# Kernel tuning notes

Measured on AMD Instinct MI355X. Metric: run time of the kernel, lower is better.

Reference implementation:

```python
import jax, jax.numpy as jnp
import numpy as np

N, E, D = 50000, 1200000, 64
NEG_SLOPE = 0.2  # PyG GATConv LeakyReLU slope
EPS_SM = 1e-16   # PyG softmax eps
EPS_LN = 1e-5


def _glorot(key, shape):
    fan = shape[0]
    return jax.random.normal(key, shape, jnp.float32) / np.float32(np.sqrt(fan))


def setup_inputs() -> dict:
    key = jax.random.key(0)
    ks = jax.random.split(key, 16)
    inp = {
        "x": jax.random.normal(ks[0], (N, D), jnp.float32),
        "edge_index": jax.random.randint(ks[1], (2, E), 0, N, dtype=jnp.int32),
        # layer 0: bipartite-style (-1,-1) GATConv -> separate src/dst projections
        "W_src0": _glorot(ks[2], (D, D)), "W_dst0": _glorot(ks[3], (D, D)),
        "a_src0": _glorot(ks[4], (D,)), "a_dst0": _glorot(ks[5], (D,)),
        "b0": jnp.zeros((D,), jnp.float32),
        "lin_W0": _glorot(ks[6], (D, D)), "lin_b0": jnp.zeros((D,), jnp.float32),
        # layers 1,2: int in_channels -> shared projection for src and dst
        "W1": _glorot(ks[7], (D, D)),
        "a_src1": _glorot(ks[8], (D,)), "a_dst1": _glorot(ks[9], (D,)),
        "b1": jnp.zeros((D,), jnp.float32),
        "lin_W1": _glorot(ks[10], (D, D)), "lin_b1": jnp.zeros((D,), jnp.float32),
        "W2": _glorot(ks[11], (D, D)),
        "a_src2": _glorot(ks[12], (D,)), "a_dst2": _glorot(ks[13], (D,)),
        "b2": jnp.zeros((D,), jnp.float32),
        "lin_W2": _glorot(ks[14], (D, D)), "lin_b2": jnp.zeros((D,), jnp.float32),
        "ln_w": jnp.ones((D,), jnp.float32), "ln_b": jnp.zeros((D,), jnp.float32),
        "proj_W": _glorot(ks[15], (D, 1)), "proj_b": jnp.zeros((1,), jnp.float32),
    }
    return inp


def _gat(x_src, x_dst, a_src, a_dst, bias, src, dst):
    # per-edge attention logit: a_src.x_j + a_dst.x_i, LeakyReLU
    alpha = (x_src * a_src).sum(-1)[src] + (x_dst * a_dst).sum(-1)[dst]  # [E]
    alpha = jnp.where(alpha >= 0, alpha, NEG_SLOPE * alpha)
    # segment softmax over edges sharing a destination node
    m = jax.ops.segment_max(alpha, dst, num_segments=N)
    m = jnp.where(jnp.isfinite(m), m, 0.0)  # empty segments -> -inf -> 0
    e = jnp.exp(alpha - m[dst])
    denom = jax.ops.segment_sum(e, dst, num_segments=N)
    w = e / (denom[dst] + EPS_SM)
    # weighted scatter-add aggregation
    return jax.ops.segment_sum(w[:, None] * x_src[src], dst, num_segments=N) + bias


def reference(x, edge_index,
              W_src0, W_dst0, a_src0, a_dst0, b0, lin_W0, lin_b0,
              W1, a_src1, a_dst1, b1, lin_W1, lin_b1,
              W2, a_src2, a_dst2, b2, lin_W2, lin_b2,
              ln_w, ln_b, proj_W, proj_b):
    src, dst = edge_index[0], edge_index[1]
    h = _gat(x @ W_src0, x @ W_dst0, a_src0, a_dst0, b0, src, dst) + x @ lin_W0 + lin_b0
    h = jax.nn.relu(h)
    hp = h @ W1
    h = _gat(hp, hp, a_src1, a_dst1, b1, src, dst) + h @ lin_W1 + lin_b1
    h = jax.nn.relu(h)
    hp = h @ W2
    h = _gat(hp, hp, a_src2, a_dst2, b2, src, dst) + h @ lin_W2 + lin_b2
    # PyG LayerNorm mode='graph': normalize over all nodes and channels
    mu = h.mean()
    var = h.var()
    h = (h - mu) * jax.lax.rsqrt(var + EPS_LN) * ln_w + ln_b
    return h @ proj_W + proj_b  # [N, 1]
```

## Files before the change

### kernel.cpp

```cpp
#include <hip/hip_runtime.h>
#include <hip/hip_bf16.h>

#define NN 50000
#define NE 1200000
#define D 64
#define NEG_SLOPE 0.2f
#define EPS_SM 1e-16f
#define EPS_LN 1e-5f
#define KMAX 4
#define PIPE 8
#define BSH 6
#define NBUK 782
#define BCAP 2048
#define BCAPSH 11
#define EPB 4096
#define NPB 293
#define GEMM_BLOCKS 3125
#define GAT_BLOCKS 12500

typedef __attribute__((ext_vector_type(8))) short short8;
typedef __attribute__((ext_vector_type(4))) float float4v;

__device__ __forceinline__ float waveReduceSum(float v) {
    #pragma unroll
    for (int off = 32; off > 0; off >>= 1)
        v += __shfl_xor(v, off, 64);
    return v;
}
__device__ __forceinline__ float bflo(unsigned v) { return __uint_as_float(v << 16); }
__device__ __forceinline__ float bfhi(unsigned v) { return __uint_as_float(v & 0xffff0000u); }
__device__ __forceinline__ short f2bf_bits(float f) {
    __hip_bfloat16 b = __float2bfloat16(f);
    short v; __builtin_memcpy(&v, &b, 2);
    return v;
}

struct WP7 { const float* p[7]; };

__global__ __launch_bounds__(256) void pack_w7(WP7 wp, unsigned short* __restrict__ wpk) {
    const int n = 7 * 4096;
    for (int idx = blockIdx.x * 256 + threadIdx.x; idx < n; idx += gridDim.x * 256) {
        const int j = idx & 7;
        const int lane = (idx >> 3) & 63;
        const int khtile = idx >> 9;
        const int kh = khtile & 1;
        const int tile = khtile >> 1;
        const int mat = tile >> 2;
        const int ch = (tile & 3) * 16 + (lane & 15);
        const int k = kh * 32 + (lane >> 4) * 8 + j;
        wpk[idx] = (unsigned short)f2bf_bits(wp.p[mat][k * D + ch]);
    }
}

template <int NMATS>
__global__ __launch_bounds__(256) void gemm_mfma(
                          const float* __restrict__ hin,
                          const unsigned short* __restrict__ wpk,
                          const float* __restrict__ avs,
                          const float* __restrict__ avd,
                          const float* __restrict__ bgat,
                          const float* __restrict__ blin,
                          __hip_bfloat16* __restrict__ hp,
                          float* __restrict__ agg,
                          float* __restrict__ alpha_s,
                          float* __restrict__ alpha_d) {
    constexpr int NT   = NMATS * 4;
    constexpr int NTPW = NT / 4;
    __shared__ float xt[16 * D];
    __shared__ float ared[2][4][16];

    const int t   = threadIdx.x;
    const int nb0 = blockIdx.x * 16;
    ((float4*)xt)[t] = ((const float4*)(hin + (size_t)nb0 * D))[t];
    __syncthreads();

    const int w    = t >> 6;
    const int lane = t & 63;
    const int mrow = lane & 15;
    const int kq   = lane >> 4;

    short8 a[2];
    #pragma unroll
    for (int kh = 0; kh < 2; ++kh) {
        const float* xp = xt + mrow * D + kh * 32 + kq * 8;
        const float4 f0 = *(const float4*)(xp);
        const float4 f1 = *(const float4*)(xp + 4);
        a[kh][0] = f2bf_bits(f0.x); a[kh][1] = f2bf_bits(f0.y);
        a[kh][2] = f2bf_bits(f0.z); a[kh][3] = f2bf_bits(f0.w);
        a[kh][4] = f2bf_bits(f1.x); a[kh][5] = f2bf_bits(f1.y);
        a[kh][6] = f2bf_bits(f1.z); a[kh][7] = f2bf_bits(f1.w);
    }

    float4v acc[NTPW];
    #pragma unroll
    for (int i = 0; i < NTPW; ++i) {
        const int tile = w * NTPW + i;
        const short8 b0 = *(const short8*)(wpk + ((size_t)(tile * 2 + 0) * 64 + lane) * 8);
        const short8 b1 = *(const short8*)(wpk + ((size_t)(tile * 2 + 1) * 64 + lane) * 8);
        float4v c = {0.f, 0.f, 0.f, 0.f};
        c = __builtin_amdgcn_mfma_f32_16x16x32_bf16(a[0], b0, c, 0, 0, 0);
        c = __builtin_amdgcn_mfma_f32_16x16x32_bf16(a[1], b1, c, 0, 0, 0);
        acc[i] = c;
    }

    float psr[4] = {0.f, 0.f, 0.f, 0.f};
    float pdr[4] = {0.f, 0.f, 0.f, 0.f};
    #pragma unroll
    for (int i = 0; i < NTPW; ++i) {
        const int tile = w * NTPW + i;
        const int mat  = tile >> 2;
        const int c64  = (tile & 3) * 16 + mrow;
        const float av_s = avs[c64], av_d = avd[c64];
        const float bias = blin[c64] + bgat[c64];
        #pragma unroll
        for (int r = 0; r < 4; ++r) {
            const int node = nb0 + kq * 4 + r;
            const float v = acc[i][r];
            if (mat == 0) {
                hp[(size_t)node * D + c64] = __float2bfloat16(v);
                psr[r] += v * av_s;
                if (NMATS == 2) pdr[r] += v * av_d;
            } else if (NMATS == 3 && mat == 1) {
                pdr[r] += v * av_d;
            } else {
                agg[(size_t)node * D + c64] = v + bias;
            }
        }
    }
    #pragma unroll
    for (int off = 1; off < 16; off <<= 1) {
        #pragma unroll
        for (int r = 0; r < 4; ++r) {
            psr[r] += __shfl_xor(psr[r], off, 64);
            pdr[r] += __shfl_xor(pdr[r], off, 64);
        }
    }
    if (mrow == 0) {
        #pragma unroll
        for (int r = 0; r < 4; ++r) {
            ared[0][w][kq * 4 + r] = psr[r];
            ared[1][w][kq * 4 + r] = pdr[r];
        }
    }
    __syncthreads();
    if (t < 16) {
        alpha_s[nb0 + t] = ared[0][0][t] + ared[0][1][t] + ared[0][2][t] + ared[0][3][t];
        alpha_d[nb0 + t] = ared[1][0][t] + ared[1][1][t] + ared[1][2][t] + ared[1][3][t];
    }
}

__global__ __launch_bounds__(256) void bucket_partition(const int* __restrict__ ei,
                                                        int* __restrict__ bcur,
                                                        int* __restrict__ pairs) {
    __shared__ int h[NBUK];
    __shared__ int cur[NBUK];
    for (int i = threadIdx.x; i < NBUK; i += 256) h[i] = 0;
    __syncthreads();
    const int base = blockIdx.x * EPB;
    const int lim  = min(EPB, NE - base);
    for (int i = threadIdx.x; i < lim; i += 256)
        atomicAdd(&h[ei[NE + base + i] >> BSH], 1);
    __syncthreads();
    for (int i = threadIdx.x; i < NBUK; i += 256) {
        const int c = h[i];
        cur[i] = c ? atomicAdd(&bcur[i], c) : 0;
    }
    __syncthreads();
    for (int i = threadIdx.x; i < lim; i += 256) {
        const int s = ei[base + i];
        const int d = ei[NE + base + i];
        const int b = d >> BSH;
        const int pos = atomicAdd(&cur[b], 1);
        if (pos < BCAP) pairs[(b << BCAPSH) + pos] = s | ((d & 63) << 16);
    }
}

__global__ __launch_bounds__(256) void csr_finalize(const int* __restrict__ pairs,
                                                    const int* __restrict__ bcur,
                                                    int* __restrict__ cnt,
                                                    int* __restrict__ row_start,
                                                    int* __restrict__ csr_src) {
    __shared__ int ncnt[64];
    __shared__ int lsrc[BCAP];
    const int t = threadIdx.x;
    const int b = blockIdx.x;
    const int beg = b << BCAPSH;
    const int m = min(bcur[b], BCAP);
    const int nbase = b << BSH;
    if (t < 64) ncnt[t] = 0;
    __syncthreads();
    for (int i = t; i < m; i += 256)
        atomicAdd(&ncnt[pairs[beg + i] >> 16], 1);
    __syncthreads();
    if (t < 64) {
        const int v = ncnt[t];
        int inc = v;
        #pragma unroll
        for (int off = 1; off < 64; off <<= 1) {
            const int u = __shfl_up(inc, off, 64);
            if (t >= off) inc += u;
        }
        const int excl = inc - v;
        if (nbase + t < NN) {
            cnt[nbase + t] = v;
            row_start[nbase + t] = beg + excl;
        }
        ncnt[t] = excl;
    }
    __syncthreads();
    for (int i = t; i < m; i += 256) {
        const int p = pairs[beg + i];
        const int pos = atomicAdd(&ncnt[p >> 16], 1);
        lsrc[pos] = p & 0xffff;
    }
    __syncthreads();
    for (int i = t; i < m; i += 256)
        csr_src[beg + i] = lsrc[i];
}

template <bool DO_RELU, bool DO_STATS>
__global__ __launch_bounds__(256) void gat_node(
                         const int* __restrict__ csr_src,
                         const int* __restrict__ row_start,
                         const int* __restrict__ cnt,
                         const float* __restrict__ as,
                         const float* __restrict__ ad,
                         const __hip_bfloat16* __restrict__ hp,
                         float* __restrict__ agg,
                         float* __restrict__ partial) {
    __shared__ int2 esm[4][KMAX * 64];
    const int wv   = threadIdx.x >> 6;
    const int lane = threadIdx.x & 63;
    const int node = blockIdx.x * 4 + wv;
    const int snode = __builtin_amdgcn_readfirstlane(node);
    const int deg = cnt[snode];
    const int rs  = row_start[snode];
    const int half = lane >> 5;
    const int c2   = lane & 31;
    float2 acc = make_float2(0.f, 0.f);
    if (deg > 0) {
        const float ad_d = ad[snode];
        int   sr[KMAX];
        float ea[KMAX];
        float sum = 0.f;
        #pragma unroll
        for (int k = 0; k < KMAX; ++k) {
            const int j = k * 64 + lane;
            const bool valid = j < deg;
            const int s = valid ? __builtin_nontemporal_load(csr_src + rs + j) : 0;
            float a = valid ? (as[s] + ad_d) : 0.f;
            a = (a >= 0.f) ? a : NEG_SLOPE * a;
            float e = valid ? __expf(a) : 0.f;
            sr[k] = s;
            ea[k] = e;
            sum += e;
        }
        sum = waveReduceSum(sum);
        const float inv = 1.f / (sum + EPS_SM);
        #pragma unroll
        for (int k = 0; k < KMAX; ++k)
            esm[wv][k * 64 + lane] = make_int2(sr[k] * 32, __float_as_int(ea[k] * inv));
        const unsigned* hp32 = (const unsigned*)hp;
        const int T    = (deg + 1) >> 1;
        const int Tpad = (T + PIPE - 1) & ~(PIPE - 1);
        int2     pp[PIPE];
        unsigned vv[PIPE];
        #pragma unroll
        for (int i = 0; i < PIPE; ++i) {
            const int2 p = esm[wv][2 * i + half];
            pp[i] = p;
            vv[i] = hp32[p.x + c2];
        }
        float2 a0 = make_float2(0.f, 0.f), a1 = make_float2(0.f, 0.f);
        for (int t0 = 0; t0 + PIPE < Tpad; t0 += PIPE) {
            #pragma unroll
            for (int i = 0; i < PIPE; ++i) {
                const float    w = __int_as_float(pp[i].y);
                const unsigned v = vv[i];
                const int2 np = esm[wv][2 * (t0 + PIPE + i) + half];
                pp[i] = np;
                vv[i] = hp32[np.x + c2];
                if (i & 1) {
                    a1.x = fmaf(w, bflo(v), a1.x);
                    a1.y = fmaf(w, bfhi(v), a1.y);
                } else {
                    a0.x = fmaf(w, bflo(v), a0.x);
                    a0.y = fmaf(w, bfhi(v), a0.y);
                }
            }
        }
        #pragma unroll
        for (int i = 0; i < PIPE; ++i) {
            const float w = __int_as_float(pp[i].y);
            if (i & 1) {
                a1.x = fmaf(w, bflo(vv[i]), a1.x);
                a1.y = fmaf(w, bfhi(vv[i]), a1.y);
            } else {
                a0.x = fmaf(w, bflo(vv[i]), a0.x);
                a0.y = fmaf(w, bfhi(vv[i]), a0.y);
            }
        }
        acc.x = a0.x + a1.x;
        acc.y = a0.y + a1.y;
    }
    acc.x += __shfl_xor(acc.x, 32, 64);
    acc.y += __shfl_xor(acc.y, 32, 64);

    float2 r2 = make_float2(0.f, 0.f);
    if (half == 0) {
        const float2 g = *(const float2*)(agg + (size_t)node * D + 2 * c2);
        r2.x = g.x + acc.x;
        r2.y = g.y + acc.y;
        if (DO_RELU) { r2.x = fmaxf(r2.x, 0.f); r2.y = fmaxf(r2.y, 0.f); }
        *(float2*)(agg + (size_t)node * D + 2 * c2) = r2;
    }
    if (DO_STATS) {
        float s  = r2.x + r2.y;
        float ss = r2.x * r2.x + r2.y * r2.y;
        s  = waveReduceSum(s);
        ss = waveReduceSum(ss);
        __shared__ float red[2][4];
        if (lane == 0) { red[0][wv] = s; red[1][wv] = ss; }
        __syncthreads();
        if (threadIdx.x == 0) {
            partial[blockIdx.x]              = red[0][0] + red[0][1] + red[0][2] + red[0][3];
            partial[GAT_BLOCKS + blockIdx.x] = red[1][0] + red[1][1] + red[1][2] + red[1][3];
        }
    }
}

__global__ void ln_reduce(const float* __restrict__ partial, float* __restrict__ stats) {
    float s = 0.f, ss = 0.f;
    for (int i = threadIdx.x; i < GAT_BLOCKS; i += 256) {
        s  += partial[i];
        ss += partial[GAT_BLOCKS + i];
    }
    s  = waveReduceSum(s);
    ss = waveReduceSum(ss);
    __shared__ float sm[2][4];
    if ((threadIdx.x & 63) == 0) {
        sm[0][threadIdx.x >> 6] = s;
        sm[1][threadIdx.x >> 6] = ss;
    }
    __syncthreads();
    if (threadIdx.x == 0) {
        stats[0] = sm[0][0] + sm[0][1] + sm[0][2] + sm[0][3];
        stats[1] = sm[1][0] + sm[1][1] + sm[1][2] + sm[1][3];
    }
}

__global__ void finalize(const float* __restrict__ x,
                         const float* __restrict__ stats,
                         const float* __restrict__ lnw,
                         const float* __restrict__ lnb,
                         const float* __restrict__ pw,
                         const float* __restrict__ pb,
                         float* __restrict__ out) {
    const int wave = (blockIdx.x * blockDim.x + threadIdx.x) >> 6;
    const int lane = threadIdx.x & 63;
    if (wave >= NN) return;
    const float inv_nd = 1.f / (float)(NN * D);
    const float mu  = stats[0] * inv_nd;
    const float var = stats[1] * inv_nd - mu * mu;
    const float rs = rsqrtf(var + EPS_LN);
    const float v = x[(size_t)wave * D + lane];
    const float xn = (v - mu) * rs * lnw[lane] + lnb[lane];
    const float c = waveReduceSum(xn * pw[lane]);
    if (lane == 0) out[wave] = c + pb[0];
}

extern "C" void kernel_launch(void* const* d_in, const int* in_sizes, int n_in,
                              void* d_out, int out_size, void* d_ws, size_t ws_size,
                              hipStream_t stream) {
    const float* x     = (const float*)d_in[0];
    const int*   ei    = (const int*)d_in[1];
    const float* Wsrc0 = (const float*)d_in[2];
    const float* Wdst0 = (const float*)d_in[3];
    const float* asrc0 = (const float*)d_in[4];
    const float* adst0 = (const float*)d_in[5];
    const float* b0    = (const float*)d_in[6];
    const float* linW0 = (const float*)d_in[7];
    const float* linb0 = (const float*)d_in[8];
    const float* W1    = (const float*)d_in[9];
    const float* asrc1 = (const float*)d_in[10];
    const float* adst1 = (const float*)d_in[11];
    const float* b1    = (const float*)d_in[12];
    const float* linW1 = (const float*)d_in[13];
    const float* linb1 = (const float*)d_in[14];
    const float* W2    = (const float*)d_in[15];
    const float* asrc2 = (const float*)d_in[16];
    const float* adst2 = (const float*)d_in[17];
    const float* b2    = (const float*)d_in[18];
    const float* linW2 = (const float*)d_in[19];
    const float* linb2 = (const float*)d_in[20];
    const float* lnw   = (const float*)d_in[21];
    const float* lnb   = (const float*)d_in[22];
    const float* pW    = (const float*)d_in[23];
    const float* pb    = (const float*)d_in[24];
    float* out = (float*)d_out;

    int*  csr_src   = (int*)d_ws;
    int*  cnt       = csr_src + NBUK * BCAP;
    int*  row_start = cnt + NN;
    int*  bcur      = row_start + NN;
    size_t off = (size_t)(NBUK * BCAP + 2 * NN + NBUK);
    off = (off + 3) & ~(size_t)3;
    float* A     = (float*)d_ws + off;
    int*   pairs = (int*)A;
    float* B     = A + (size_t)NN * D;
    __hip_bfloat16* P = (__hip_bfloat16*)(B + NN * D);
    float* alpha_s = (float*)(P + NN * D);
    float* alpha_d = alpha_s + NN;
    float* stats   = alpha_d + NN;
    float* partial = stats + 2;
    unsigned short* wpk = (unsigned short*)(((uintptr_t)(partial + 2 * GAT_BLOCKS) + 15) & ~(uintptr_t)15);

    const int elem_blocks = (NN * D) / 256;

    WP7 wp = {{Wsrc0, Wdst0, linW0, W1, linW1, W2, linW2}};
    pack_w7<<<112, 256, 0, stream>>>(wp, wpk);
    hipMemsetAsync(bcur, 0, NBUK * sizeof(int), stream);
    bucket_partition<<<NPB, 256, 0, stream>>>(ei, bcur, pairs);
    csr_finalize<<<NBUK, 256, 0, stream>>>(pairs, bcur, cnt, row_start, csr_src);

    gemm_mfma<3><<<GEMM_BLOCKS, 256, 0, stream>>>(x, wpk, asrc0, adst0, b0, linb0,
                                                  P, A, alpha_s, alpha_d);
    gat_node<true, false><<<GAT_BLOCKS, 256, 0, stream>>>(csr_src, row_start, cnt,
                                                          alpha_s, alpha_d, P, A, partial);

    gemm_mfma<2><<<GEMM_BLOCKS, 256, 0, stream>>>(A, wpk + 3 * 4096, asrc1, adst1, b1, linb1,
                                                  P, B, alpha_s, alpha_d);
    gat_node<true, false><<<GAT_BLOCKS, 256, 0, stream>>>(csr_src, row_start, cnt,
                                                          alpha_s, alpha_d, P, B, partial);

    gemm_mfma<2><<<GEMM_BLOCKS, 256, 0, stream>>>(B, wpk + 5 * 4096, asrc2, adst2, b2, linb2,
                                                  P, A, alpha_s, alpha_d);
    gat_node<false, true><<<GAT_BLOCKS, 256, 0, stream>>>(csr_src, row_start, cnt,
                                                          alpha_s, alpha_d, P, A, partial);

    ln_reduce<<<1, 256, 0, stream>>>(partial, stats);
    finalize<<<elem_blocks, 256, 0, stream>>>(A, stats, lnw, lnb, pW, pb, out);
}
```

Measured before the change: 319.0 us.

## Split bf16 feature table into channel halves and aggregate each half separately

The GEMM now writes the projected bf16 features as two planar halves of 32 channels each. The GAT aggregation kernel is launched twice per layer, once per half. Each half-table is 3.2 MB, so its gathered rows are more likely to stay in L2 cache, and each wave gathers four edges per iteration using 16 lanes per edge. The cost is that every launch repeats the softmax and logit work, each layer has twice as many launches, and the reads become 64-byte row segments.

```diff
diff --git a/kernel.cpp b/kernel.cpp
--- a/kernel.cpp
+++ b/kernel.cpp
@@ -117,7 +117,9 @@
             const int node = nb0 + kq * 4 + r;
             const float v = acc[i][r];
             if (mat == 0) {
-                hp[(size_t)node * D + c64] = __float2bfloat16(v);
+                const int hhalf = c64 >> 5;
+                const int hc    = c64 & 31;
+                hp[(size_t)hhalf * NN * 32 + (size_t)node * 32 + hc] = __float2bfloat16(v);
                 psr[r] += v * av_s;
                 if (NMATS == 2) pdr[r] += v * av_d;
             } else if (NMATS == 3 && mat == 1) {
@@ -227,7 +229,8 @@
                          const float* __restrict__ ad,
                          const __hip_bfloat16* __restrict__ hp,
                          float* __restrict__ agg,
-                         float* __restrict__ partial) {
+                         float* __restrict__ partial,
+                         const int half) {
     __shared__ int2 esm[4][KMAX * 64];
     const int wv   = threadIdx.x >> 6;
     const int lane = threadIdx.x & 63;
@@ -235,8 +238,9 @@
     const int snode = __builtin_amdgcn_readfirstlane(node);
     const int deg = cnt[snode];
     const int rs  = row_start[snode];
-    const int half = lane >> 5;
-    const int c2   = lane & 31;
+    const int g   = lane >> 4;
+    const int cl  = lane & 15;
+    const unsigned* hph = (const unsigned*)hp + (size_t)half * NN * 16;
     float2 acc = make_float2(0.f, 0.f);
     if (deg > 0) {
         const float ad_d = ad[snode];
@@ -259,17 +263,16 @@
         const float inv = 1.f / (sum + EPS_SM);
         #pragma unroll
         for (int k = 0; k < KMAX; ++k)
-            esm[wv][k * 64 + lane] = make_int2(sr[k] * 32, __float_as_int(ea[k] * inv));
-        const unsigned* hp32 = (const unsigned*)hp;
-        const int T    = (deg + 1) >> 1;
+            esm[wv][k * 64 + lane] = make_int2(sr[k] * 16, __float_as_int(ea[k] * inv));
+        const int T    = (deg + 3) >> 2;
         const int Tpad = (T + PIPE - 1) & ~(PIPE - 1);
         int2     pp[PIPE];
         unsigned vv[PIPE];
         #pragma unroll
         for (int i = 0; i < PIPE; ++i) {
-            const int2 p = esm[wv][2 * i + half];
+            const int2 p = esm[wv][4 * i + g];
             pp[i] = p;
-            vv[i] = hp32[p.x + c2];
+            vv[i] = hph[p.x + cl];
         }
         float2 a0 = make_float2(0.f, 0.f), a1 = make_float2(0.f, 0.f);
         for (int t0 = 0; t0 + PIPE < Tpad; t0 += PIPE) {
@@ -277,9 +280,9 @@
             for (int i = 0; i < PIPE; ++i) {
                 const float    w = __int_as_float(pp[i].y);
                 const unsigned v = vv[i];
-                const int2 np = esm[wv][2 * (t0 + PIPE + i) + half];
+                const int2 np = esm[wv][4 * (t0 + PIPE + i) + g];
                 pp[i] = np;
-                vv[i] = hp32[np.x + c2];
+                vv[i] = hph[np.x + cl];
                 if (i & 1) {
                     a1.x = fmaf(w, bflo(v), a1.x);
                     a1.y = fmaf(w, bfhi(v), a1.y);
@@ -303,16 +306,19 @@
         acc.x = a0.x + a1.x;
         acc.y = a0.y + a1.y;
     }
-    acc.x += __shfl_xor(acc.x, 32, 64);
-    acc.y += __shfl_xor(acc.y, 32, 64);
+    #pragma unroll
+    for (int off = 16; off < 64; off <<= 1) {
+        acc.x += __shfl_xor(acc.x, off, 64);
+        acc.y += __shfl_xor(acc.y, off, 64);
+    }
 
     float2 r2 = make_float2(0.f, 0.f);
-    if (half == 0) {
-        const float2 g = *(const float2*)(agg + (size_t)node * D + 2 * c2);
-        r2.x = g.x + acc.x;
-        r2.y = g.y + acc.y;
+    if (lane < 16) {
+        const float2 gv = *(const float2*)(agg + (size_t)node * D + half * 32 + 2 * lane);
+        r2.x = gv.x + acc.x;
+        r2.y = gv.y + acc.y;
         if (DO_RELU) { r2.x = fmaxf(r2.x, 0.f); r2.y = fmaxf(r2.y, 0.f); }
-        *(float2*)(agg + (size_t)node * D + 2 * c2) = r2;
+        *(float2*)(agg + (size_t)node * D + half * 32 + 2 * lane) = r2;
     }
     if (DO_STATS) {
         float s  = r2.x + r2.y;
@@ -323,17 +329,18 @@
         if (lane == 0) { red[0][wv] = s; red[1][wv] = ss; }
         __syncthreads();
         if (threadIdx.x == 0) {
-            partial[blockIdx.x]              = red[0][0] + red[0][1] + red[0][2] + red[0][3];
-            partial[GAT_BLOCKS + blockIdx.x] = red[1][0] + red[1][1] + red[1][2] + red[1][3];
+            const int slot = half * GAT_BLOCKS + blockIdx.x;
+            partial[slot]                  = red[0][0] + red[0][1] + red[0][2] + red[0][3];
+            partial[2 * GAT_BLOCKS + slot] = red[1][0] + red[1][1] + red[1][2] + red[1][3];
         }
     }
 }
 
 __global__ void ln_reduce(const float* __restrict__ partial, float* __restrict__ stats) {
     float s = 0.f, ss = 0.f;
-    for (int i = threadIdx.x; i < GAT_BLOCKS; i += 256) {
+    for (int i = threadIdx.x; i < 2 * GAT_BLOCKS; i += 256) {
         s  += partial[i];
-        ss += partial[GAT_BLOCKS + i];
+        ss += partial[2 * GAT_BLOCKS + i];
     }
     s  = waveReduceSum(s);
     ss = waveReduceSum(ss);
@@ -413,7 +420,7 @@
     float* alpha_d = alpha_s + NN;
     float* stats   = alpha_d + NN;
     float* partial = stats + 2;
-    unsigned short* wpk = (unsigned short*)(((uintptr_t)(partial + 2 * GAT_BLOCKS) + 15) & ~(uintptr_t)15);
+    unsigned short* wpk = (unsigned short*)(((uintptr_t)(partial + 4 * GAT_BLOCKS) + 15) & ~(uintptr_t)15);
 
     const int elem_blocks = (NN * D) / 256;
 
@@ -426,17 +433,23 @@
     gemm_mfma<3><<<GEMM_BLOCKS, 256, 0, stream>>>(x, wpk, asrc0, adst0, b0, linb0,
                                                   P, A, alpha_s, alpha_d);
     gat_node<true, false><<<GAT_BLOCKS, 256, 0, stream>>>(csr_src, row_start, cnt,
-                                                          alpha_s, alpha_d, P, A, partial);
+                                                          alpha_s, alpha_d, P, A, partial, 0);
+    gat_node<true, false><<<GAT_BLOCKS, 256, 0, stream>>>(csr_src, row_start, cnt,
+                                                          alpha_s, alpha_d, P, A, partial, 1);
 
     gemm_mfma<2><<<GEMM_BLOCKS, 256, 0, stream>>>(A, wpk + 3 * 4096, asrc1, adst1, b1, linb1,
                                                   P, B, alpha_s, alpha_d);
     gat_node<true, false><<<GAT_BLOCKS, 256, 0, stream>>>(csr_src, row_start, cnt,
-                                                          alpha_s, alpha_d, P, B, partial);
+                                                          alpha_s, alpha_d, P, B, partial, 0);
+    gat_node<true, false><<<GAT_BLOCKS, 256, 0, stream>>>(csr_src, row_start, cnt,
+                                                          alpha_s, alpha_d, P, B, partial, 1);
 
     gemm_mfma<2><<<GEMM_BLOCKS, 256, 0, stream>>>(B, wpk + 5 * 4096, asrc2, adst2, b2, linb2,
                                                   P, A, alpha_s, alpha_d);
     gat_node<false, true><<<GAT_BLOCKS, 256, 0, stream>>>(csr_src, row_start, cnt,
-                                                          alpha_s, alpha_d, P, A, partial);
+                                                          alpha_s, alpha_d, P, A, partial, 0);
+    gat_node<false, true><<<GAT_BLOCKS, 256, 0, stream>>>(csr_src, row_start, cnt,
+                                                          alpha_s, alpha_d, P, A, partial, 1);
 
     ln_reduce<<<1, 256, 0, stream>>>(partial, stats);
     finalize<<<elem_blocks, 256, 0, stream>>>(A, stats, lnw, lnb, pW, pb, out);
```

After: 379.6 us. +19.0%, slower.
